# Optimization experiments

Hardware: AMD Instinct MI355X
Metric: run time of the kernel (lower is better)

The kernel has to match this reference:

```python
import jax, jax.numpy as jnp
import numpy as np

B, C, X = 64, 2, 262144
H = 256          # hidden_dim
K = 8            # max_fronts
THR = 1e-06      # diff_threshold
LN_EPS = 1e-5


def _layernorm(x, g, b):
    mu = jnp.mean(x, axis=-1, keepdims=True)
    var = jnp.var(x, axis=-1, keepdims=True)
    return (x - mu) * jax.lax.rsqrt(var + LN_EPS) * g + b


def setup_inputs() -> dict:
    key = jax.random.key(0)
    ks = jax.random.split(key, 16)
    density = jax.random.normal(ks[0], (B, X), dtype=jnp.float32)
    coords = jnp.broadcast_to(jnp.linspace(0.0, 1.0, X, dtype=jnp.float32), (B, X))
    x = jnp.stack([density, coords], axis=1)  # (B, 2, X)

    def lin(k, fan_in, shape):
        return jax.random.normal(k, shape, dtype=jnp.float32) * (1.0 / np.sqrt(fan_in))

    inp = {
        "x": x,
        # input_proj: Linear(6, H) + LayerNorm(H)
        "w_in": lin(ks[1], 6, (6, H)),
        "b_in": jnp.zeros((H,), jnp.float32),
        "ln_in_g": jnp.ones((H,), jnp.float32),
        "ln_in_b": jnp.zeros((H,), jnp.float32),
        # 3 residual blocks, stacked on leading axis
        "rb_ln_g": jnp.ones((3, H), jnp.float32),
        "rb_ln_b": jnp.zeros((3, H), jnp.float32),
        "rb_w1": lin(ks[2], H, (3, H, 2 * H)),
        "rb_b1": jnp.zeros((3, 2 * H), jnp.float32),
        "rb_w2": lin(ks[3], 2 * H, (3, 2 * H, H)),
        "rb_b2": jnp.zeros((3, H), jnp.float32),
        # output head: LayerNorm(H) -> Linear(H, H//2) -> GELU -> Linear(H//2, 2)
        "out_ln_g": jnp.ones((H,), jnp.float32),
        "out_ln_b": jnp.zeros((H,), jnp.float32),
        "out_w1": lin(ks[4], H, (H, H // 2)),
        "out_b1": jnp.zeros((H // 2,), jnp.float32),
        "out_w2": lin(ks[5], H // 2, (H // 2, 2)),
        "out_b2": jnp.zeros((2,), jnp.float32),
    }
    return inp


def _speed_predictor(uL, uR, w_in, b_in, ln_in_g, ln_in_b,
                     rb_ln_g, rb_ln_b, rb_w1, rb_b1, rb_w2, rb_b2,
                     out_ln_g, out_ln_b, out_w1, out_b1, out_w2, out_b2):
    diff = uL - uR
    feats = jnp.stack([uL, uR, diff, jnp.abs(diff), (uL + uR) * 0.5,
                       jnp.sign(diff)], axis=-1)          # (B, K, 6)
    h = jax.nn.gelu(_layernorm(feats @ w_in + b_in, ln_in_g, ln_in_b),
                    approximate=False)                    # (B, K, H)
    for i in range(3):  # fixed small layer loop
        z = _layernorm(h, rb_ln_g[i], rb_ln_b[i])
        z = jax.nn.gelu(z @ rb_w1[i] + rb_b1[i], approximate=False)
        h = h + (z @ rb_w2[i] + rb_b2[i])
    z = _layernorm(h, out_ln_g, out_ln_b)
    z = jax.nn.gelu(z @ out_w1 + out_b1, approximate=False)
    return z @ out_w2 + out_b2                            # (B, K, 2)


def reference(x, w_in, b_in, ln_in_g, ln_in_b,
              rb_ln_g, rb_ln_b, rb_w1, rb_b1, rb_w2, rb_b2,
              out_ln_g, out_ln_b, out_w1, out_b1, out_w2, out_b2):
    density = x[:, 0, :]
    coords = x[:, -1, :]
    left_vals, right_vals = density[:, :-1], density[:, 1:]
    has_disc = jnp.abs(left_vals - right_vals) > THR       # (B, X-1)
    all_fc = (coords[:, :-1] + coords[:, 1:]) * 0.5        # (B, X-1)
    front_count = jnp.sum(has_disc, axis=-1)               # (B,)
    score = jnp.where(has_disc, all_fc, jnp.inf)
    # smallest-K coords -> top_k of negated score (K <= X-1 here)
    _, idx = jax.lax.top_k(-score, K)                      # (B, K)
    uL = jnp.take_along_axis(left_vals, idx, axis=-1)
    uR = jnp.take_along_axis(right_vals, idx, axis=-1)
    fc = jnp.take_along_axis(all_fc, idx, axis=-1)
    valid = jnp.take_along_axis(has_disc, idx, axis=-1).astype(x.dtype)
    speed = _speed_predictor(uL, uR, w_in, b_in, ln_in_g, ln_in_b,
                             rb_ln_g, rb_ln_b, rb_w1, rb_b1, rb_w2, rb_b2,
                             out_ln_g, out_ln_b, out_w1, out_b1, out_w2, out_b2)
    front_params = jnp.concatenate(
        [jnp.transpose(speed, (0, 2, 1)),                  # (B, 2, K)
         uL[:, None], uR[:, None], fc[:, None], valid[:, None]], axis=1)
    return front_params, front_count
```

## Files before the change

kernel.cpp:

```cpp
#include <hip/hip_runtime.h>
#include <hip/hip_bf16.h>
#include <math.h>

#define XN 262144
#define NPAIR (XN - 1)
#define BN 64
#define HD 256
#define KK 8
#define THRC 1e-6f

__device__ __forceinline__ float gelu_f(float x) {
    return 0.5f * x * (1.0f + erff(x * 0.70710678118654752440f));
}

__global__ __launch_bounds__(256) void count_select_kernel(
    const float* __restrict__ x, float* __restrict__ out,
    float* __restrict__ ws_uLuR, int* __restrict__ ws_cnt) {
    __shared__ int sred[4];
    const int b = blockIdx.x >> 4;
    const int p = blockIdx.x & 15;
    const float* row = x + (size_t)b * 2 * XN;
    const int tid = threadIdx.x;
    const int lane = tid & 63, wave = tid >> 6;

    if (p == 0 && tid < 64) {
        const float* c = row + XN;
        int idxs[KK];
        float vflag[KK];
        int found = 0;
        for (int base = 0; base < NPAIR && found < KK; base += 64) {
            int i = base + lane;
            bool v = (i < NPAIR) && (fabsf(row[i] - row[i + 1]) > THRC);
            unsigned long long m = __ballot(v);
            while (m && found < KK) {
                int l = __ffsll(m) - 1;
                idxs[found] = base + l;
                vflag[found] = 1.0f;
                ++found;
                m &= (m - 1);
            }
        }
        if (found < KK) {
            for (int base = 0; base < NPAIR && found < KK; base += 64) {
                int i = base + lane;
                bool v = (i < NPAIR) && !(fabsf(row[i] - row[i + 1]) > THRC);
                unsigned long long m = __ballot(v);
                while (m && found < KK) {
                    int l = __ffsll(m) - 1;
                    idxs[found] = base + l;
                    vflag[found] = 0.0f;
                    ++found;
                    m &= (m - 1);
                }
            }
        }
        if (lane < KK) {
            int i = idxs[lane];
            float uL = row[i];
            float uR = row[i + 1];
            float fc = (c[i] + c[i + 1]) * 0.5f;
            float* o = out + b * 48;
            o[16 + lane] = uL;
            o[24 + lane] = uR;
            o[32 + lane] = fc;
            o[40 + lane] = vflag[lane];
            ws_uLuR[(b * KK + lane) * 2 + 0] = uL;
            ws_uLuR[(b * KK + lane) * 2 + 1] = uR;
        }
    }

    int cnt = 0;
    const int base0 = p * 16384;
#pragma unroll
    for (int it = 0; it < 16; ++it) {
        int e0 = base0 + ((it << 8) + tid) * 4;
        float4 f = *(const float4*)(row + e0);
        cnt += (fabsf(f.x - f.y) > THRC);
        cnt += (fabsf(f.y - f.z) > THRC);
        cnt += (fabsf(f.z - f.w) > THRC);
        if (e0 + 4 < XN) {
            float e = row[e0 + 4];
            cnt += (fabsf(f.w - e) > THRC);
        }
    }
#pragma unroll
    for (int off = 32; off > 0; off >>= 1) cnt += __shfl_down(cnt, off, 64);
    if (lane == 0) sred[wave] = cnt;
    __syncthreads();
    if (tid == 0) ws_cnt[blockIdx.x] = sred[0] + sred[1] + sred[2] + sred[3];
}


#define FMA4x2(a0, a1, w4, z2v)              \
    a0.x = fmaf(w4.x, z2v.x, a0.x);          \
    a0.y = fmaf(w4.y, z2v.x, a0.y);          \
    a0.z = fmaf(w4.z, z2v.x, a0.z);          \
    a0.w = fmaf(w4.w, z2v.x, a0.w);          \
    a1.x = fmaf(w4.x, z2v.y, a1.x);          \
    a1.y = fmaf(w4.y, z2v.y, a1.y);          \
    a1.z = fmaf(w4.z, z2v.y, a1.z);          \
    a1.w = fmaf(w4.w, z2v.y, a1.w);

__global__ __launch_bounds__(512) void mlp_kernel(
    const float* __restrict__ ws_uLuR, const int* __restrict__ ws_cnt,
    const float* __restrict__ w_in, const float* __restrict__ b_in,
    const float* __restrict__ ln_in_g, const float* __restrict__ ln_in_b,
    const float* __restrict__ rb_ln_g, const float* __restrict__ rb_ln_b,
    const float* __restrict__ rb_w1, const float* __restrict__ rb_b1,
    const float* __restrict__ rb_w2, const float* __restrict__ rb_b2,
    const float* __restrict__ out_ln_g, const float* __restrict__ out_ln_b,
    const float* __restrict__ out_w1, const float* __restrict__ out_b1,
    const float* __restrict__ out_w2, const float* __restrict__ out_b2,
    float* __restrict__ out) {
    __shared__ float2 hsv[HD];
    __shared__ float2 ztv[HD];
    __shared__ float2 z2tv[2 * HD];
    __shared__ float2 z3tv[HD / 2];
    __shared__ float part[4096];
    __shared__ float red[8][2][2];
    __shared__ float stat[2][2];
    __shared__ float fin[2][4];

    const int tid = threadIdx.x;
    const int bid = blockIdx.x;
    const int b = bid >> 2;
    const int sub = bid & 3;
    const int wave = tid >> 6, lane = tid & 63;

    if (sub == 0 && wave == 0) {
        int v = (lane < 16) ? ws_cnt[b * 16 + lane] : 0;
#pragma unroll
        for (int off = 8; off > 0; off >>= 1) v += __shfl_down(v, off, 64);
        if (lane == 0) out[3072 + b] = (float)v;
    }

    if (tid < HD) {
        const int c = tid;
        float fw[6];
#pragma unroll
        for (int f = 0; f < 6; ++f) fw[f] = w_in[f * HD + c];
        float bin = b_in[c];
        float2 hv;
        float* hvp = (float*)&hv;
#pragma unroll
        for (int j = 0; j < 2; ++j) {
            int tok = b * KK + sub * 2 + j;
            float uL = ws_uLuR[tok * 2 + 0];
            float uR = ws_uLuR[tok * 2 + 1];
            float dd = uL - uR;
            float sg = (dd > 0.0f) ? 1.0f : ((dd < 0.0f) ? -1.0f : 0.0f);
            hvp[j] = bin + uL * fw[0] + uR * fw[1] + dd * fw[2] +
                     fabsf(dd) * fw[3] + (uL + uR) * 0.5f * fw[4] + sg * fw[5];
        }
        hsv[c] = hv;
    }
    __syncthreads();

#define LN_STATS()                                                            \
    do {                                                                      \
        if (tid < HD) {                                                       \
            float2 h2 = hsv[tid];                                             \
            float s[2] = {h2.x, h2.y};                                        \
            float q[2] = {h2.x * h2.x, h2.y * h2.y};                          \
            for (int off = 32; off > 0; off >>= 1) {                          \
                _Pragma("unroll") for (int j = 0; j < 2; ++j) {               \
                    s[j] += __shfl_down(s[j], off, 64);                       \
                    q[j] += __shfl_down(q[j], off, 64);                       \
                }                                                             \
            }                                                                 \
            if (lane == 0) {                                                  \
                _Pragma("unroll") for (int j = 0; j < 2; ++j) {               \
                    red[wave][j][0] = s[j];                                   \
                    red[wave][j][1] = q[j];                                   \
                }                                                             \
            }                                                                 \
        }                                                                     \
        __syncthreads();                                                      \
        if (tid < 2) {                                                        \
            float ts = 0.0f, tq = 0.0f;                                       \
            _Pragma("unroll") for (int w = 0; w < 4; ++w) {                   \
                ts += red[w][tid][0];                                         \
                tq += red[w][tid][1];                                         \
            }                                                                 \
            float mu = ts * (1.0f / 256.0f);                                  \
            float vr = tq * (1.0f / 256.0f) - mu * mu;                        \
            stat[tid][0] = mu;                                                \
            stat[tid][1] = rsqrtf(vr + 1e-5f);                                \
        }                                                                     \
        __syncthreads();                                                      \
    } while (0)

    LN_STATS();
    if (tid < HD) {
        const int c = tid;
        float g = ln_in_g[c], be = ln_in_b[c];
        float2 hv = hsv[c];
        hv.x = gelu_f((hv.x - stat[0][0]) * stat[0][1] * g + be);
        hv.y = gelu_f((hv.y - stat[1][0]) * stat[1][1] * g + be);
        hsv[c] = hv;
    }
    __syncthreads();

    for (int i = 0; i < 3; ++i) {
        LN_STATS();
        if (tid < HD) {
            const int c = tid;
            float gg = rb_ln_g[i * HD + c], bb = rb_ln_b[i * HD + c];
            float2 hv = hsv[c], zv;
            zv.x = (hv.x - stat[0][0]) * stat[0][1] * gg + bb;
            zv.y = (hv.y - stat[1][0]) * stat[1][1] * gg + bb;
            ztv[c] = zv;
        }
        __syncthreads();

        {
            const float* w1 = rb_w1 + (size_t)i * HD * 2 * HD;
            const int cg = tid & 127, kh = tid >> 7;
            const float* wp = w1 + (size_t)(kh * 64) * (2 * HD) + cg * 4;
            float4 a0 = {0, 0, 0, 0}, a1 = {0, 0, 0, 0};
#pragma unroll 8
            for (int k = 0; k < 64; ++k) {
                float4 w4 = *(const float4*)wp;
                wp += 2 * HD;
                float2 z2v = ztv[kh * 64 + k];
                FMA4x2(a0, a1, w4, z2v);
            }
            float* pp = part + (kh * 128 + cg) * 8;
            *(float4*)(pp + 0) = a0;
            *(float4*)(pp + 4) = a1;
        }
        __syncthreads();
        {
            const int c2 = tid;
            const int cg = c2 >> 2, c = c2 & 3;
            float b1v = rb_b1[i * 2 * HD + c2];
            float2 zv;
#pragma unroll
            for (int j = 0; j < 2; ++j) {
                int o = cg * 8 + j * 4 + c;
                float v = b1v + part[o] + part[o + 1024] + part[o + 2048] +
                          part[o + 3072];
                ((float*)&zv)[j] = gelu_f(v);
            }
            z2tv[c2] = zv;
        }
        __syncthreads();

        {
            const float* w2 = rb_w2 + (size_t)i * 2 * HD * HD;
            const int cg2 = tid & 63, kh2 = tid >> 6;
            const float* wp = w2 + (size_t)(kh2 * 64) * HD + cg2 * 4;
            float4 a0 = {0, 0, 0, 0}, a1 = {0, 0, 0, 0};
#pragma unroll 8
            for (int k = 0; k < 64; ++k) {
                float4 w4 = *(const float4*)wp;
                wp += HD;
                float2 z2v = z2tv[kh2 * 64 + k];
                FMA4x2(a0, a1, w4, z2v);
            }
            float* pp = part + (kh2 * 64 + cg2) * 8;
            *(float4*)(pp + 0) = a0;
            *(float4*)(pp + 4) = a1;
        }
        __syncthreads();
        if (tid < HD) {
            const int c2 = tid;
            const int cg2 = c2 >> 2, c = c2 & 3;
            float b2v = rb_b2[i * HD + c2];
            float2 hv = hsv[c2];
#pragma unroll
            for (int j = 0; j < 2; ++j) {
                int o = cg2 * 8 + j * 4 + c;
                float v = b2v;
#pragma unroll
                for (int kh = 0; kh < 8; ++kh) v += part[o + kh * 512];
                ((float*)&hv)[j] += v;
            }
            hsv[c2] = hv;
        }
        __syncthreads();
    }

    LN_STATS();
    if (tid < HD) {
        const int c = tid;
        float gg = out_ln_g[c], bb = out_ln_b[c];
        float2 hv = hsv[c], zv;
        zv.x = (hv.x - stat[0][0]) * stat[0][1] * gg + bb;
        zv.y = (hv.y - stat[1][0]) * stat[1][1] * gg + bb;
        ztv[c] = zv;
    }
    __syncthreads();

    {
        const int cg3 = tid & 31, kh3 = tid >> 5;
        const float* wp = out_w1 + (size_t)(kh3 * 16) * (HD / 2) + cg3 * 4;
        float4 a0 = {0, 0, 0, 0}, a1 = {0, 0, 0, 0};
#pragma unroll 4
        for (int k = 0; k < 16; ++k) {
            float4 w4 = *(const float4*)wp;
            wp += HD / 2;
            float2 z2v = ztv[kh3 * 16 + k];
            FMA4x2(a0, a1, w4, z2v);
        }
        float* pp = part + (kh3 * 32 + cg3) * 8;
        *(float4*)(pp + 0) = a0;
        *(float4*)(pp + 4) = a1;
    }
    __syncthreads();
    if (tid < HD / 2) {
        const int c2 = tid;
        const int cg3 = c2 >> 2, c = c2 & 3;
        float bv = out_b1[c2];
        float2 zv;
#pragma unroll
        for (int j = 0; j < 2; ++j) {
            int o = cg3 * 8 + j * 4 + c;
            float v = bv;
#pragma unroll
            for (int kh = 0; kh < 16; ++kh) v += part[o + kh * 256];
            ((float*)&zv)[j] = gelu_f(v);
        }
        z3tv[c2] = zv;
    }
    __syncthreads();

    if (tid < HD / 2) {
        float2 z = z3tv[tid];
        float w0 = out_w2[tid * 2 + 0];
        float w1v = out_w2[tid * 2 + 1];
        float p[4];
        p[0] = z.x * w0; p[1] = z.x * w1v;
        p[2] = z.y * w0; p[3] = z.y * w1v;
#pragma unroll
        for (int off = 32; off > 0; off >>= 1) {
#pragma unroll
            for (int u = 0; u < 4; ++u) p[u] += __shfl_down(p[u], off, 64);
        }
        if (lane == 0) {
#pragma unroll
            for (int u = 0; u < 4; ++u) fin[wave][u] = p[u];
        }
    }
    __syncthreads();
    if (tid < 4) {
        int j = tid >> 1;
        int o = tid & 1;
        float s = out_b2[o] + fin[0][tid] + fin[1][tid];
        out[b * 48 + o * 8 + sub * 2 + j] = s;
    }
}

extern "C" void kernel_launch(void* const* d_in, const int* in_sizes, int n_in,
                              void* d_out, int out_size, void* d_ws, size_t ws_size,
                              hipStream_t stream) {
    const float* x        = (const float*)d_in[0];
    const float* w_in     = (const float*)d_in[1];
    const float* b_in     = (const float*)d_in[2];
    const float* ln_in_g  = (const float*)d_in[3];
    const float* ln_in_b  = (const float*)d_in[4];
    const float* rb_ln_g  = (const float*)d_in[5];
    const float* rb_ln_b  = (const float*)d_in[6];
    const float* rb_w1    = (const float*)d_in[7];
    const float* rb_b1    = (const float*)d_in[8];
    const float* rb_w2    = (const float*)d_in[9];
    const float* rb_b2    = (const float*)d_in[10];
    const float* out_ln_g = (const float*)d_in[11];
    const float* out_ln_b = (const float*)d_in[12];
    const float* out_w1   = (const float*)d_in[13];
    const float* out_b1   = (const float*)d_in[14];
    const float* out_w2   = (const float*)d_in[15];
    const float* out_b2   = (const float*)d_in[16];

    float* out = (float*)d_out;
    float* wsf = (float*)d_ws;
    int* wsc = (int*)(wsf + 1024);

    count_select_kernel<<<BN * 16, 256, 0, stream>>>(x, out, wsf, wsc);
    mlp_kernel<<<BN * 4, 512, 0, stream>>>(
        wsf, wsc, w_in, b_in, ln_in_g, ln_in_b, rb_ln_g, rb_ln_b,
        rb_w1, rb_b1, rb_w2, rb_b2, out_ln_g, out_ln_b,
        out_w1, out_b1, out_w2, out_b2, out);
}
```

Before: 260.1 us.

## Convert MLP weights to bf16 in a prep kernel and stream them in mlp_kernel

Adds a conversion kernel that rounds the residual-block and output-head weight matrices to bf16 in workspace on every call. The MLP kernel then reads 8 bf16 weights per 16-byte load and unpacks them to fp32 for the FMAs. This halves weight traffic per block, since each of the 256 blocks re-reads about 3 MB of weights. Work is repartitioned to 8 columns per thread over more k-slices, with a larger shared partial-sum buffer. It adds an extra launch and precision loss in the weights, which may affect tolerance.

Result: faster. 245.7 us (-5.5%).

```diff
diff --git a/kernel.cpp b/kernel.cpp
--- a/kernel.cpp
+++ b/kernel.cpp
@@ -11,6 +11,28 @@
 
 __device__ __forceinline__ float gelu_f(float x) {
     return 0.5f * x * (1.0f + erff(x * 0.70710678118654752440f));
+}
+
+__device__ __forceinline__ unsigned short f2bf(float f) {
+    unsigned int x = __float_as_uint(f);
+    unsigned int r = (x + 0x7fffu + ((x >> 16) & 1u)) >> 16;
+    return (unsigned short)r;
+}
+
+__global__ __launch_bounds__(256) void convert_kernel(
+    const float* __restrict__ rb_w1, const float* __restrict__ rb_w2,
+    const float* __restrict__ out_w1, unsigned short* __restrict__ bw) {
+    int t = blockIdx.x * 256 + threadIdx.x;
+    const float* s;
+    if (t < 49152) s = rb_w1 + (size_t)t * 8;
+    else if (t < 98304) s = rb_w2 + (size_t)(t - 49152) * 8;
+    else s = out_w1 + (size_t)(t - 98304) * 8;
+    float4 a = *(const float4*)s;
+    float4 b = *(const float4*)(s + 4);
+    union { unsigned short u[8]; uint4 v; } r;
+    r.u[0] = f2bf(a.x); r.u[1] = f2bf(a.y); r.u[2] = f2bf(a.z); r.u[3] = f2bf(a.w);
+    r.u[4] = f2bf(b.x); r.u[5] = f2bf(b.y); r.u[6] = f2bf(b.z); r.u[7] = f2bf(b.w);
+    *(uint4*)(bw + (size_t)t * 8) = r.v;
 }
 
 __global__ __launch_bounds__(256) void count_select_kernel(
@@ -91,32 +113,43 @@
 }
 
 
-#define FMA4x2(a0, a1, w4, z2v)              \
-    a0.x = fmaf(w4.x, z2v.x, a0.x);          \
-    a0.y = fmaf(w4.y, z2v.x, a0.y);          \
-    a0.z = fmaf(w4.z, z2v.x, a0.z);          \
-    a0.w = fmaf(w4.w, z2v.x, a0.w);          \
-    a1.x = fmaf(w4.x, z2v.y, a1.x);          \
-    a1.y = fmaf(w4.y, z2v.y, a1.y);          \
-    a1.z = fmaf(w4.z, z2v.y, a1.z);          \
-    a1.w = fmaf(w4.w, z2v.y, a1.w);
+#define BF8_FMA(w, z)                                                        \
+    do {                                                                     \
+        float f0, f1;                                                        \
+        f0 = __uint_as_float((w).x << 16);                                   \
+        f1 = __uint_as_float((w).x & 0xffff0000u);                           \
+        a0[0] = fmaf(f0, (z).x, a0[0]); a1[0] = fmaf(f0, (z).y, a1[0]);      \
+        a0[1] = fmaf(f1, (z).x, a0[1]); a1[1] = fmaf(f1, (z).y, a1[1]);      \
+        f0 = __uint_as_float((w).y << 16);                                   \
+        f1 = __uint_as_float((w).y & 0xffff0000u);                           \
+        a0[2] = fmaf(f0, (z).x, a0[2]); a1[2] = fmaf(f0, (z).y, a1[2]);      \
+        a0[3] = fmaf(f1, (z).x, a0[3]); a1[3] = fmaf(f1, (z).y, a1[3]);      \
+        f0 = __uint_as_float((w).z << 16);                                   \
+        f1 = __uint_as_float((w).z & 0xffff0000u);                           \
+        a0[4] = fmaf(f0, (z).x, a0[4]); a1[4] = fmaf(f0, (z).y, a1[4]);      \
+        a0[5] = fmaf(f1, (z).x, a0[5]); a1[5] = fmaf(f1, (z).y, a1[5]);      \
+        f0 = __uint_as_float((w).w << 16);                                   \
+        f1 = __uint_as_float((w).w & 0xffff0000u);                           \
+        a0[6] = fmaf(f0, (z).x, a0[6]); a1[6] = fmaf(f0, (z).y, a1[6]);      \
+        a0[7] = fmaf(f1, (z).x, a0[7]); a1[7] = fmaf(f1, (z).y, a1[7]);      \
+    } while (0)
 
 __global__ __launch_bounds__(512) void mlp_kernel(
     const float* __restrict__ ws_uLuR, const int* __restrict__ ws_cnt,
+    const unsigned short* __restrict__ bw,
     const float* __restrict__ w_in, const float* __restrict__ b_in,
     const float* __restrict__ ln_in_g, const float* __restrict__ ln_in_b,
     const float* __restrict__ rb_ln_g, const float* __restrict__ rb_ln_b,
-    const float* __restrict__ rb_w1, const float* __restrict__ rb_b1,
-    const float* __restrict__ rb_w2, const float* __restrict__ rb_b2,
+    const float* __restrict__ rb_b1, const float* __restrict__ rb_b2,
     const float* __restrict__ out_ln_g, const float* __restrict__ out_ln_b,
-    const float* __restrict__ out_w1, const float* __restrict__ out_b1,
+    const float* __restrict__ out_b1,
     const float* __restrict__ out_w2, const float* __restrict__ out_b2,
     float* __restrict__ out) {
     __shared__ float2 hsv[HD];
     __shared__ float2 ztv[HD];
     __shared__ float2 z2tv[2 * HD];
     __shared__ float2 z3tv[HD / 2];
-    __shared__ float part[4096];
+    __shared__ float part[8192];
     __shared__ float red[8][2][2];
     __shared__ float stat[2][2];
     __shared__ float fin[2][4];
@@ -214,69 +247,79 @@
         __syncthreads();
 
         {
-            const float* w1 = rb_w1 + (size_t)i * HD * 2 * HD;
-            const int cg = tid & 127, kh = tid >> 7;
-            const float* wp = w1 + (size_t)(kh * 64) * (2 * HD) + cg * 4;
-            float4 a0 = {0, 0, 0, 0}, a1 = {0, 0, 0, 0};
+            const unsigned short* w1 = bw + (size_t)i * (HD * 2 * HD);
+            const int cg = tid & 63, kh = tid >> 6;
+            const unsigned short* wp = w1 + (size_t)(kh * 32) * (2 * HD) + cg * 8;
+            float a0[8] = {0, 0, 0, 0, 0, 0, 0, 0};
+            float a1[8] = {0, 0, 0, 0, 0, 0, 0, 0};
 #pragma unroll 8
-            for (int k = 0; k < 64; ++k) {
-                float4 w4 = *(const float4*)wp;
+            for (int k = 0; k < 32; ++k) {
+                uint4 w = *(const uint4*)wp;
                 wp += 2 * HD;
-                float2 z2v = ztv[kh * 64 + k];
-                FMA4x2(a0, a1, w4, z2v);
-            }
-            float* pp = part + (kh * 128 + cg) * 8;
-            *(float4*)(pp + 0) = a0;
-            *(float4*)(pp + 4) = a1;
+                float2 z = ztv[kh * 32 + k];
+                BF8_FMA(w, z);
+            }
+            float* pp = part + (kh * 64 + cg) * 16;
+#pragma unroll
+            for (int u = 0; u < 8; ++u) {
+                pp[u * 2] = a0[u];
+                pp[u * 2 + 1] = a1[u];
+            }
         }
         __syncthreads();
         {
             const int c2 = tid;
-            const int cg = c2 >> 2, c = c2 & 3;
-            float b1v = rb_b1[i * 2 * HD + c2];
+            const int cg = c2 >> 3, u = c2 & 7;
+            float vx = rb_b1[i * 2 * HD + c2];
+            float vy = vx;
+#pragma unroll
+            for (int kh = 0; kh < 8; ++kh) {
+                const float* pp = part + (kh * 64 + cg) * 16 + u * 2;
+                vx += pp[0];
+                vy += pp[1];
+            }
             float2 zv;
-#pragma unroll
-            for (int j = 0; j < 2; ++j) {
-                int o = cg * 8 + j * 4 + c;
-                float v = b1v + part[o] + part[o + 1024] + part[o + 2048] +
-                          part[o + 3072];
-                ((float*)&zv)[j] = gelu_f(v);
-            }
+            zv.x = gelu_f(vx);
+            zv.y = gelu_f(vy);
             z2tv[c2] = zv;
         }
         __syncthreads();
 
         {
-            const float* w2 = rb_w2 + (size_t)i * 2 * HD * HD;
-            const int cg2 = tid & 63, kh2 = tid >> 6;
-            const float* wp = w2 + (size_t)(kh2 * 64) * HD + cg2 * 4;
-            float4 a0 = {0, 0, 0, 0}, a1 = {0, 0, 0, 0};
+            const unsigned short* w2 = bw + 393216 + (size_t)i * (2 * HD * HD);
+            const int cg2 = tid & 31, kh2 = tid >> 5;
+            const unsigned short* wp = w2 + (size_t)(kh2 * 32) * HD + cg2 * 8;
+            float a0[8] = {0, 0, 0, 0, 0, 0, 0, 0};
+            float a1[8] = {0, 0, 0, 0, 0, 0, 0, 0};
 #pragma unroll 8
-            for (int k = 0; k < 64; ++k) {
-                float4 w4 = *(const float4*)wp;
+            for (int k = 0; k < 32; ++k) {
+                uint4 w = *(const uint4*)wp;
                 wp += HD;
-                float2 z2v = z2tv[kh2 * 64 + k];
-                FMA4x2(a0, a1, w4, z2v);
-            }
-            float* pp = part + (kh2 * 64 + cg2) * 8;
-            *(float4*)(pp + 0) = a0;
-            *(float4*)(pp + 4) = a1;
+                float2 z = z2tv[kh2 * 32 + k];
+                BF8_FMA(w, z);
+            }
+            float* pp = part + (kh2 * 32 + cg2) * 16;
+#pragma unroll
+            for (int u = 0; u < 8; ++u) {
+                pp[u * 2] = a0[u];
+                pp[u * 2 + 1] = a1[u];
+            }
         }
         __syncthreads();
         if (tid < HD) {
-            const int c2 = tid;
-            const int cg2 = c2 >> 2, c = c2 & 3;
-            float b2v = rb_b2[i * HD + c2];
-            float2 hv = hsv[c2];
-#pragma unroll
-            for (int j = 0; j < 2; ++j) {
-                int o = cg2 * 8 + j * 4 + c;
-                float v = b2v;
-#pragma unroll
-                for (int kh = 0; kh < 8; ++kh) v += part[o + kh * 512];
-                ((float*)&hv)[j] += v;
-            }
-            hsv[c2] = hv;
+            const int cg2 = tid >> 3, u = tid & 7;
+            float vx = rb_b2[i * HD + tid];
+            float vy = vx;
+#pragma unroll
+            for (int kh = 0; kh < 16; ++kh) {
+                const float* pp = part + (kh * 32 + cg2) * 16 + u * 2;
+                vx += pp[0];
+                vy += pp[1];
+            }
+            float2 hv = hsv[tid];
+            hv.x += vx;
+            hv.y += vy;
+            hsv[tid] = hv;
         }
         __syncthreads();
     }
@@ -293,35 +336,40 @@
     __syncthreads();
 
     {
-        const int cg3 = tid & 31, kh3 = tid >> 5;
-        const float* wp = out_w1 + (size_t)(kh3 * 16) * (HD / 2) + cg3 * 4;
-        float4 a0 = {0, 0, 0, 0}, a1 = {0, 0, 0, 0};
-#pragma unroll 4
-        for (int k = 0; k < 16; ++k) {
-            float4 w4 = *(const float4*)wp;
+        const unsigned short* ow1 = bw + 786432;
+        const int cg3 = tid & 15, kh3 = tid >> 4;
+        const unsigned short* wp = ow1 + (size_t)(kh3 * 8) * (HD / 2) + cg3 * 8;
+        float a0[8] = {0, 0, 0, 0, 0, 0, 0, 0};
+        float a1[8] = {0, 0, 0, 0, 0, 0, 0, 0};
+#pragma unroll
+        for (int k = 0; k < 8; ++k) {
+            uint4 w = *(const uint4*)wp;
             wp += HD / 2;
-            float2 z2v = ztv[kh3 * 16 + k];
-            FMA4x2(a0, a1, w4, z2v);
-        }
-        float* pp = part + (kh3 * 32 + cg3) * 8;
-        *(float4*)(pp + 0) = a0;
-        *(float4*)(pp + 4) = a1;
+            float2 z = ztv[kh3 * 8 + k];
+            BF8_FMA(w, z);
+        }
+        float* pp = part + (kh3 * 16 + cg3) * 16;
+#pragma unroll
+        for (int u = 0; u < 8; ++u) {
+            pp[u * 2] = a0[u];
+            pp[u * 2 + 1] = a1[u];
+        }
     }
     __syncthreads();
     if (tid < HD / 2) {
-        const int c2 = tid;
-        const int cg3 = c2 >> 2, c = c2 & 3;
-        float bv = out_b1[c2];
+        const int cg3 = tid >> 3, u = tid & 7;
+        float vx = out_b1[tid];
+        float vy = vx;
+#pragma unroll
+        for (int kh = 0; kh < 32; ++kh) {
+            const float* pp = part + (kh * 16 + cg3) * 16 + u * 2;
+            vx += pp[0];
+            vy += pp[1];
+        }
         float2 zv;
-#pragma unroll
-        for (int j = 0; j < 2; ++j) {
-            int o = cg3 * 8 + j * 4 + c;
-            float v = bv;
-#pragma unroll
-            for (int kh = 0; kh < 16; ++kh) v += part[o + kh * 256];
-            ((float*)&zv)[j] = gelu_f(v);
-        }
-        z3tv[c2] = zv;
+        zv.x = gelu_f(vx);
+        zv.y = gelu_f(vy);
+        z3tv[tid] = zv;
     }
     __syncthreads();
 
@@ -375,10 +423,11 @@
     float* out = (float*)d_out;
     float* wsf = (float*)d_ws;
     int* wsc = (int*)(wsf + 1024);
-
+    unsigned short* bw = (unsigned short*)(wsf + 2048);
+
+    convert_kernel<<<400, 256, 0, stream>>>(rb_w1, rb_w2, out_w1, bw);
     count_select_kernel<<<BN * 16, 256, 0, stream>>>(x, out, wsf, wsc);
     mlp_kernel<<<BN * 4, 512, 0, stream>>>(
-        wsf, wsc, w_in, b_in, ln_in_g, ln_in_b, rb_ln_g, rb_ln_b,
-        rb_w1, rb_b1, rb_w2, rb_b2, out_ln_g, out_ln_b,
-        out_w1, out_b1, out_w2, out_b2, out);
-}
+        wsf, wsc, bw, w_in, b_in, ln_in_g, ln_in_b, rb_ln_g, rb_ln_b,
+        rb_b1, rb_b2, out_ln_g, out_ln_b, out_b1, out_w2, out_b2, out);
+}
```
